# Kernel tuning notes

Hardware: AMD Instinct MI355X
Metric: run time of the kernel (lower is better)

The kernel has to match this reference:

```python
import jax, jax.numpy as jnp
import numpy as np

N_NODES = 100000


def _deg_inv_sqrt(dst, num_nodes):
    # degree with self-loops (PyG GCNConv default: add_self_loops=True)
    deg = jax.ops.segment_sum(jnp.ones(dst.shape[0], jnp.float32), dst,
                              num_segments=num_nodes) + 1.0
    return jax.lax.rsqrt(deg)


def gcn_conv(x, W, b, src, dst, dis, num_nodes):
    # PyG GCNConv: h = X W; out = D^-1/2 (A + I) D^-1/2 h + b
    h = x @ W                                  # [N, F_out]
    norm = dis[src] * dis[dst]                 # [E]
    msg = h[src] * norm[:, None]               # [E, F_out] (gather)
    out = jax.ops.segment_sum(msg, dst, num_segments=num_nodes)  # scatter-add
    out = out + h * (dis * dis)[:, None]       # self-loop contribution
    return out + b


def setup_inputs() -> dict:
    key = jax.random.key(0)
    ks = jax.random.split(key, 6)
    n, e = N_NODES, 1600000
    in_f, hid_f, out_f = 64, 64, 32
    x = jax.random.normal(ks[0], (n, in_f), jnp.float32)
    edge_index = jax.random.randint(ks[1], (2, e), 0, n, jnp.int64)
    s1 = 1.0 / np.sqrt(in_f)
    s2 = 1.0 / np.sqrt(hid_f)
    W1 = jax.random.normal(ks[2], (in_f, hid_f), jnp.float32) * s1
    b1 = jnp.zeros((hid_f,), jnp.float32)
    W2 = jax.random.normal(ks[3], (hid_f, out_f), jnp.float32) * s2
    b2 = jnp.zeros((out_f,), jnp.float32)
    return {"x": x, "edge_index": edge_index, "W1": W1, "b1": b1,
            "W2": W2, "b2": b2}


def reference(x, edge_index, W1, b1, W2, b2):
    src, dst = edge_index[0], edge_index[1]
    dis = _deg_inv_sqrt(dst, N_NODES)
    h = gcn_conv(x, W1, b1, src, dst, dis, N_NODES)
    h = jax.nn.relu(h)
    return gcn_conv(h, W2, b2, src, dst, dis, N_NODES)
```

## Files before the change

### kernel.cpp

```cpp
#include <hip/hip_runtime.h>
#include <hip/hip_bf16.h>


constexpr int N = 100000;
constexpr int E = 1600000;
constexpr int NBINS = 1563;
constexpr int HB    = 1568;
constexpr int CAP   = 1536;
constexpr int P1B   = 391;
constexpr int GB    = 1563;

__global__ void __launch_bounds__(256) fused_pass1_gemm1(
    const float* __restrict__ x, const float* __restrict__ W1,
    __hip_bfloat16* __restrict__ h1u,
    const int* __restrict__ src, const int* __restrict__ dst,
    int* __restrict__ cursor, unsigned* __restrict__ rec) {
    __shared__ float ws[64][64];
    __shared__ float xsT[64][64];
    const int bid = blockIdx.x;
    const int t = threadIdx.x;
    if (bid < P1B) {
        int* hist  = (int*)ws;
        int* rbase = hist + HB;
        int* rcur  = rbase + HB;
        for (int i = t; i < HB; i += 256) hist[i] = 0;
        __syncthreads();
        int myd[16], mys[16];
        const int e0 = bid * 4096;
#pragma unroll
        for (int it = 0; it < 16; ++it) {
            int idx = e0 + it * 256 + t;
            bool ok = idx < E;
            myd[it] = ok ? dst[idx] : -1;
            mys[it] = ok ? src[idx] : 0;
            if (ok) atomicAdd(&hist[myd[it] >> 6], 1);
        }
        __syncthreads();
        for (int i = t; i < HB; i += 256) {
            int h = hist[i];
            rbase[i] = (h > 0) ? atomicAdd(&cursor[i], h) : 0;
            rcur[i] = 0;
        }
        __syncthreads();
#pragma unroll
        for (int it = 0; it < 16; ++it) {
            if (myd[it] >= 0) {
                int cb = myd[it] >> 6;
                int r = atomicAdd(&rcur[cb], 1);
                int pos = rbase[cb] + r;
                if (pos < CAP)
                    rec[(size_t)cb * CAP + pos] =
                        ((unsigned)mys[it] << 6) | ((unsigned)myd[it] & 63u);
            }
        }
    } else {
        const int row0 = (bid - P1B) * 64;
        for (int i = t * 4; i < 64 * 64; i += 1024) {
            float4 v = *(const float4*)(W1 + i);
            ws[i >> 6][i & 63]       = v.x;
            ws[i >> 6][(i & 63) + 1] = v.y;
            ws[i >> 6][(i & 63) + 2] = v.z;
            ws[i >> 6][(i & 63) + 3] = v.w;
        }
        {
            const int r  = t & 63;
            const int k0 = (t >> 6) * 16;
            const int gr = row0 + r;
            if (gr < N) {
#pragma unroll
                for (int kk = 0; kk < 16; kk += 4) {
                    float4 v = *(const float4*)(x + (size_t)gr * 64 + k0 + kk);
                    xsT[k0 + kk][r]     = v.x;
                    xsT[k0 + kk + 1][r] = v.y;
                    xsT[k0 + kk + 2][r] = v.z;
                    xsT[k0 + kk + 3][r] = v.w;
                }
            } else {
#pragma unroll
                for (int kk = 0; kk < 16; ++kk) xsT[k0 + kk][r] = 0.0f;
            }
        }
        __syncthreads();
        const int c4 = (t & 15) * 4;
        const int r4 = (t >> 4) * 4;
        float acc[4][4];
#pragma unroll
        for (int i = 0; i < 4; ++i)
#pragma unroll
            for (int j = 0; j < 4; ++j) acc[i][j] = 0.0f;
#pragma unroll 4
        for (int k = 0; k < 64; ++k) {
            float4 wv = *(const float4*)&ws[k][c4];
            float4 xv = *(const float4*)&xsT[k][r4];
            float xa[4] = {xv.x, xv.y, xv.z, xv.w};
            float wa[4] = {wv.x, wv.y, wv.z, wv.w};
#pragma unroll
            for (int i = 0; i < 4; ++i)
#pragma unroll
                for (int j = 0; j < 4; ++j) acc[i][j] += xa[i] * wa[j];
        }
#pragma unroll
        for (int i = 0; i < 4; ++i) {
            const int gr = row0 + r4 + i;
            if (gr < N) {
                unsigned short o[4];
#pragma unroll
                for (int j = 0; j < 4; ++j)
                    o[j] = __bfloat16_as_ushort(__float2bfloat16(acc[i][j]));
                *(ushort4*)((unsigned short*)h1u + (size_t)gr * 64 + c4) =
                    *(const ushort4*)o;
            }
        }
    }
}

__global__ void __launch_bounds__(256) degree_kernel(
    const unsigned* __restrict__ rec, const int* __restrict__ cursor,
    float* __restrict__ dis) {
    __shared__ int cur[64];
    const int t = threadIdx.x;
    const int cb = blockIdx.x;
    if (t < 64) cur[t] = 0;
    __syncthreads();
    int m = cursor[cb];
    if (m > CAP) m = CAP;
    const unsigned* rb_ = rec + (size_t)cb * CAP;
    for (int i = t; i < m; i += 256)
        atomicAdd(&cur[rb_[i] & 63u], 1);
    __syncthreads();
    if (t < 64) {
        const int n = cb * 64 + t;
        if (n < N) dis[n] = rsqrtf((float)cur[t] + 1.0f);
    }
}

__device__ __forceinline__ void bf8_fma(float* acc, uint4 r, float w) {
    const unsigned u[4] = {r.x, r.y, r.z, r.w};
#pragma unroll
    for (int k = 0; k < 4; ++k) {
        acc[2 * k]     += __uint_as_float(u[k] << 16) * w;
        acc[2 * k + 1] += __uint_as_float(u[k] & 0xffff0000u) * w;
    }
}

__device__ __forceinline__ void bf8_acc(float* acc, uint4 r) {
    const unsigned u[4] = {r.x, r.y, r.z, r.w};
#pragma unroll
    for (int k = 0; k < 4; ++k) {
        acc[2 * k]     += __uint_as_float(u[k] << 16);
        acc[2 * k + 1] += __uint_as_float(u[k] & 0xffff0000u);
    }
}

__global__ void __launch_bounds__(512) agg1_fb(
    const __hip_bfloat16* __restrict__ h1u, const unsigned* __restrict__ rec,
    const int* __restrict__ cursor, const float* __restrict__ dis,
    const float* __restrict__ b, __hip_bfloat16* __restrict__ z1) {
    __shared__ unsigned lists[64 * 64];
    __shared__ int cur[64];
    const int t = threadIdx.x;
    const int cb = blockIdx.x;
    if (t < 64) cur[t] = 0;
    __syncthreads();
    int m = cursor[cb];
    if (m > CAP) m = CAP;
    const unsigned* rb_ = rec + (size_t)cb * CAP;
    for (int i = t; i < m; i += 512) {
        unsigned u = rb_[i];
        int dl = (int)(u & 63u);
        int r = atomicAdd(&cur[dl], 1);
        if (r < 64) lists[dl * 64 + r] = u >> 6;
    }
    __syncthreads();

    const unsigned short* hp = (const unsigned short*)h1u;
    const int row0 = cb * 64;
    const int nl = t >> 3;
    const int n = row0 + nl;
    const int fq = (t & 7) * 8;
    const int c = cur[nl];
    const int deg = (c < 64) ? c : 64;
    const unsigned* lp = &lists[nl * 64];
    float acc[8];
#pragma unroll
    for (int i = 0; i < 8; ++i) acc[i] = 0.0f;
    int j = 0;
    for (; j + 2 <= deg; j += 2) {
        unsigned s0 = lp[j], s1 = lp[j + 1];
        float w0 = dis[s0], w1 = dis[s1];
        uint4 r0 = *(const uint4*)(hp + (size_t)s0 * 64 + fq);
        uint4 r1 = *(const uint4*)(hp + (size_t)s1 * 64 + fq);
        bf8_fma(acc, r0, w0);
        bf8_fma(acc, r1, w1);
    }
    if (j < deg) {
        unsigned s0 = lp[j];
        float w0 = dis[s0];
        uint4 r0 = *(const uint4*)(hp + (size_t)s0 * 64 + fq);
        bf8_fma(acc, r0, w0);
    }
    if (n >= N) return;
    const float dn = rsqrtf((float)c + 1.0f);
    uint4 sr = *(const uint4*)(hp + (size_t)n * 64 + fq);
    bf8_fma(acc, sr, dn);
    float4 b0v = *(const float4*)(b + fq);
    float4 b1v = *(const float4*)(b + fq + 4);
    float bb[8] = {b0v.x, b0v.y, b0v.z, b0v.w, b1v.x, b1v.y, b1v.z, b1v.w};
    unsigned short o[8];
#pragma unroll
    for (int i = 0; i < 8; ++i) {
        float v = fmaxf(dn * acc[i] + bb[i], 0.0f);
        o[i] = __bfloat16_as_ushort(__float2bfloat16(v));
    }
    *(uint4*)((unsigned short*)z1 + (size_t)n * 64 + fq) = *(const uint4*)o;
}

__global__ void __launch_bounds__(256) gemm2_kernel(
    const __hip_bfloat16* __restrict__ Z, const float* __restrict__ W2,
    const float* __restrict__ dis, __hip_bfloat16* __restrict__ H2) {
    __shared__ float ws[64][32];
    __shared__ float xs[32][64];
    const int t = threadIdx.x;
    for (int i = t; i < 64 * 32; i += 256) ws[i >> 5][i & 31] = W2[i];
    const int row0 = blockIdx.x * 32;
    const unsigned short* Zp = (const unsigned short*)Z;
#pragma unroll
    for (int h = 0; h < 2; ++h) {
        int idx = h * 1024 + t * 4;
        int r = idx >> 6, k = idx & 63;
        ushort4 v = *(const ushort4*)(Zp + (size_t)(row0 + r) * 64 + k);
        xs[r][k]     = __uint_as_float((unsigned)v.x << 16);
        xs[r][k + 1] = __uint_as_float((unsigned)v.y << 16);
        xs[r][k + 2] = __uint_as_float((unsigned)v.z << 16);
        xs[r][k + 3] = __uint_as_float((unsigned)v.w << 16);
    }
    __syncthreads();
    const int c  = t & 31;
    const int rb = (t >> 5) * 4;
    float acc[4] = {0.f, 0.f, 0.f, 0.f};
    for (int k0 = 0; k0 < 64; k0 += 4) {
        float w0 = ws[k0][c], w1 = ws[k0 + 1][c];
        float w2 = ws[k0 + 2][c], w3 = ws[k0 + 3][c];
#pragma unroll
        for (int i = 0; i < 4; ++i) {
            float4 xv = *(const float4*)&xs[rb + i][k0];
            acc[i] += xv.x * w0;
            acc[i] += xv.y * w1;
            acc[i] += xv.z * w2;
            acc[i] += xv.w * w3;
        }
    }
#pragma unroll
    for (int i = 0; i < 4; ++i) {
        int row = row0 + rb + i;
        H2[(size_t)row * 32 + c] = __float2bfloat16(acc[i] * dis[row]);
    }
}

__global__ void __launch_bounds__(256) agg2_fb(
    const __hip_bfloat16* __restrict__ h2s, const unsigned* __restrict__ rec,
    const int* __restrict__ cursor, const float* __restrict__ b,
    float* __restrict__ out) {
    __shared__ unsigned lists[64 * 64];
    __shared__ int cur[64];
    const int t = threadIdx.x;
    const int cb = blockIdx.x;
    if (t < 64) cur[t] = 0;
    __syncthreads();
    int m = cursor[cb];
    if (m > CAP) m = CAP;
    const unsigned* rb_ = rec + (size_t)cb * CAP;
    for (int i = t; i < m; i += 256) {
        unsigned u = rb_[i];
        int dl = (int)(u & 63u);
        int r = atomicAdd(&cur[dl], 1);
        if (r < 64) lists[dl * 64 + r] = u >> 6;
    }
    __syncthreads();

    const unsigned short* hp = (const unsigned short*)h2s;
    const int row0 = cb * 64;
    const int nl = t >> 2;
    const int n = row0 + nl;
    const int fq = (t & 3) * 8;
    const int c = cur[nl];
    const int deg = (c < 64) ? c : 64;
    const unsigned* lp = &lists[nl * 64];
    float acc[8];
#pragma unroll
    for (int i = 0; i < 8; ++i) acc[i] = 0.0f;
    int j = 0;
    for (; j + 2 <= deg; j += 2) {
        unsigned s0 = lp[j], s1 = lp[j + 1];
        uint4 r0 = *(const uint4*)(hp + (size_t)s0 * 32 + fq);
        uint4 r1 = *(const uint4*)(hp + (size_t)s1 * 32 + fq);
        bf8_acc(acc, r0);
        bf8_acc(acc, r1);
    }
    if (j < deg) {
        unsigned s0 = lp[j];
        uint4 r0 = *(const uint4*)(hp + (size_t)s0 * 32 + fq);
        bf8_acc(acc, r0);
    }
    if (n >= N) return;
    uint4 sr = *(const uint4*)(hp + (size_t)n * 32 + fq);
    bf8_acc(acc, sr);
    const float dn = rsqrtf((float)c + 1.0f);
    float4 b0 = *(const float4*)(b + fq);
    float4 b1 = *(const float4*)(b + fq + 4);
    *(float4*)(out + (size_t)n * 32 + fq) =
        make_float4(dn * acc[0] + b0.x, dn * acc[1] + b0.y,
                    dn * acc[2] + b0.z, dn * acc[3] + b0.w);
    *(float4*)(out + (size_t)n * 32 + fq + 4) =
        make_float4(dn * acc[4] + b1.x, dn * acc[5] + b1.y,
                    dn * acc[6] + b1.z, dn * acc[7] + b1.w);
}

extern "C" void kernel_launch(void* const* d_in, const int* in_sizes, int n_in,
                              void* d_out, int out_size, void* d_ws, size_t ws_size,
                              hipStream_t stream) {
    const float* x  = (const float*)d_in[0];
    const int*   ei = (const int*)d_in[1];
    const float* W1 = (const float*)d_in[2];
    const float* b1 = (const float*)d_in[3];
    const float* W2 = (const float*)d_in[4];
    const float* b2 = (const float*)d_in[5];
    float* out = (float*)d_out;

    const int* src = ei;
    const int* dst = ei + E;

    constexpr size_t NP = 100352;
    int*      cursor = (int*)d_ws;
    float*    dis    = (float*)(cursor + 2048);
    unsigned* rec    = (unsigned*)(dis + NP);
    __hip_bfloat16* h1u = (__hip_bfloat16*)(rec + (size_t)NBINS * CAP);
    __hip_bfloat16* z1b = h1u + (size_t)N * 64;
    __hip_bfloat16* h2s = z1b + (size_t)N * 64;

    hipMemsetAsync(cursor, 0, 2048 * sizeof(int), stream);
    fused_pass1_gemm1<<<P1B + GB, 256, 0, stream>>>(x, W1, h1u, src, dst,
                                                    cursor, rec);
    degree_kernel<<<NBINS, 256, 0, stream>>>(rec, cursor, dis);
    agg1_fb<<<NBINS, 512, 0, stream>>>(h1u, rec, cursor, dis, b1, z1b);
    gemm2_kernel<<<N / 32, 256, 0, stream>>>(z1b, W2, dis, h2s);
    agg2_fb<<<NBINS, 256, 0, stream>>>(h2s, rec, cursor, b2, out);
}
```

Baseline: 185.1 us.

## Fuse layer-1 aggregation with the second GEMM into one half-bin kernel

Merges agg1 and gemm2 into one kernel. Each 256-thread block takes half of a 64-node bin, builds its neighbour lists, aggregates, applies ReLU into shared memory in fp32, then multiplies by W2 and writes the scaled bf16 h2. This removes the z1 round trip through global memory and one kernel launch. In exchange, every bin's record list is now scanned twice (once per half), and W2 is reloaded into shared memory by every block.

New measurement: 272.7 us. +47.3%, slower.

```diff
diff --git a/kernel.cpp b/kernel.cpp
--- a/kernel.cpp
+++ b/kernel.cpp
@@ -152,31 +152,40 @@
     }
 }
 
-__global__ void __launch_bounds__(512) agg1_fb(
+__global__ void __launch_bounds__(256) agg1_gemm2_half(
     const __hip_bfloat16* __restrict__ h1u, const unsigned* __restrict__ rec,
     const int* __restrict__ cursor, const float* __restrict__ dis,
-    const float* __restrict__ b, __hip_bfloat16* __restrict__ z1) {
-    __shared__ unsigned lists[64 * 64];
-    __shared__ int cur[64];
+    const float* __restrict__ b, const float* __restrict__ W2,
+    __hip_bfloat16* __restrict__ h2s) {
+    __shared__ float    ws[64][32];
+    __shared__ float    zs[32 * 68];
+    __shared__ unsigned lists[32 * 64];
+    __shared__ int      cur[32];
+    __shared__ float    dis_l[32];
     const int t = threadIdx.x;
-    const int cb = blockIdx.x;
-    if (t < 64) cur[t] = 0;
-    __syncthreads();
+    const int cb = blockIdx.x >> 1;
+    const int half = blockIdx.x & 1;
+    for (int i = t; i < 64 * 32; i += 256) ws[i >> 5][i & 31] = W2[i];
+    if (t < 32) cur[t] = 0;
+    __syncthreads();
+
     int m = cursor[cb];
     if (m > CAP) m = CAP;
     const unsigned* rb_ = rec + (size_t)cb * CAP;
-    for (int i = t; i < m; i += 512) {
+    const int hbase = half * 32;
+    for (int i = t; i < m; i += 256) {
         unsigned u = rb_[i];
-        int dl = (int)(u & 63u);
-        int r = atomicAdd(&cur[dl], 1);
-        if (r < 64) lists[dl * 64 + r] = u >> 6;
+        int dl = (int)(u & 63u) - hbase;
+        if ((unsigned)dl < 32u) {
+            int r = atomicAdd(&cur[dl], 1);
+            if (r < 64) lists[dl * 64 + r] = u >> 6;
+        }
     }
     __syncthreads();
 
     const unsigned short* hp = (const unsigned short*)h1u;
-    const int row0 = cb * 64;
     const int nl = t >> 3;
-    const int n = row0 + nl;
+    const int n = cb * 64 + hbase + nl;
     const int fq = (t & 7) * 8;
     const int c = cur[nl];
     const int deg = (c < 64) ? c : 64;
@@ -199,61 +208,48 @@
         uint4 r0 = *(const uint4*)(hp + (size_t)s0 * 64 + fq);
         bf8_fma(acc, r0, w0);
     }
-    if (n >= N) return;
-    const float dn = rsqrtf((float)c + 1.0f);
-    uint4 sr = *(const uint4*)(hp + (size_t)n * 64 + fq);
-    bf8_fma(acc, sr, dn);
-    float4 b0v = *(const float4*)(b + fq);
-    float4 b1v = *(const float4*)(b + fq + 4);
-    float bb[8] = {b0v.x, b0v.y, b0v.z, b0v.w, b1v.x, b1v.y, b1v.z, b1v.w};
-    unsigned short o[8];
-#pragma unroll
-    for (int i = 0; i < 8; ++i) {
-        float v = fmaxf(dn * acc[i] + bb[i], 0.0f);
-        o[i] = __bfloat16_as_ushort(__float2bfloat16(v));
-    }
-    *(uint4*)((unsigned short*)z1 + (size_t)n * 64 + fq) = *(const uint4*)o;
-}
-
-__global__ void __launch_bounds__(256) gemm2_kernel(
-    const __hip_bfloat16* __restrict__ Z, const float* __restrict__ W2,
-    const float* __restrict__ dis, __hip_bfloat16* __restrict__ H2) {
-    __shared__ float ws[64][32];
-    __shared__ float xs[32][64];
-    const int t = threadIdx.x;
-    for (int i = t; i < 64 * 32; i += 256) ws[i >> 5][i & 31] = W2[i];
-    const int row0 = blockIdx.x * 32;
-    const unsigned short* Zp = (const unsigned short*)Z;
-#pragma unroll
-    for (int h = 0; h < 2; ++h) {
-        int idx = h * 1024 + t * 4;
-        int r = idx >> 6, k = idx & 63;
-        ushort4 v = *(const ushort4*)(Zp + (size_t)(row0 + r) * 64 + k);
-        xs[r][k]     = __uint_as_float((unsigned)v.x << 16);
-        xs[r][k + 1] = __uint_as_float((unsigned)v.y << 16);
-        xs[r][k + 2] = __uint_as_float((unsigned)v.z << 16);
-        xs[r][k + 3] = __uint_as_float((unsigned)v.w << 16);
-    }
-    __syncthreads();
-    const int c  = t & 31;
-    const int rb = (t >> 5) * 4;
-    float acc[4] = {0.f, 0.f, 0.f, 0.f};
+    float* zr = &zs[nl * 68 + fq];
+    if (n < N) {
+        const float dn = rsqrtf((float)c + 1.0f);
+        uint4 sr = *(const uint4*)(hp + (size_t)n * 64 + fq);
+        bf8_fma(acc, sr, dn);
+        if ((t & 7) == 0) dis_l[nl] = dn;
+        float4 b0v = *(const float4*)(b + fq);
+        float4 b1v = *(const float4*)(b + fq + 4);
+        float bb[8] = {b0v.x, b0v.y, b0v.z, b0v.w, b1v.x, b1v.y, b1v.z, b1v.w};
+        float o[8];
+#pragma unroll
+        for (int i = 0; i < 8; ++i) o[i] = fmaxf(dn * acc[i] + bb[i], 0.0f);
+        *(float4*)(zr)     = make_float4(o[0], o[1], o[2], o[3]);
+        *(float4*)(zr + 4) = make_float4(o[4], o[5], o[6], o[7]);
+    } else {
+        *(float4*)(zr)     = make_float4(0.f, 0.f, 0.f, 0.f);
+        *(float4*)(zr + 4) = make_float4(0.f, 0.f, 0.f, 0.f);
+    }
+    __syncthreads();
+
+    const int cc = t & 31;
+    const int rbse = (t >> 5) * 4;
+    float oacc[4] = {0.f, 0.f, 0.f, 0.f};
     for (int k0 = 0; k0 < 64; k0 += 4) {
-        float w0 = ws[k0][c], w1 = ws[k0 + 1][c];
-        float w2 = ws[k0 + 2][c], w3 = ws[k0 + 3][c];
+        float w0 = ws[k0][cc], w1 = ws[k0 + 1][cc];
+        float w2 = ws[k0 + 2][cc], w3 = ws[k0 + 3][cc];
 #pragma unroll
         for (int i = 0; i < 4; ++i) {
-            float4 xv = *(const float4*)&xs[rb + i][k0];
-            acc[i] += xv.x * w0;
-            acc[i] += xv.y * w1;
-            acc[i] += xv.z * w2;
-            acc[i] += xv.w * w3;
+            float4 xv = *(const float4*)&zs[(rbse + i) * 68 + k0];
+            oacc[i] += xv.x * w0;
+            oacc[i] += xv.y * w1;
+            oacc[i] += xv.z * w2;
+            oacc[i] += xv.w * w3;
         }
     }
 #pragma unroll
     for (int i = 0; i < 4; ++i) {
-        int row = row0 + rb + i;
-        H2[(size_t)row * 32 + c] = __float2bfloat16(acc[i] * dis[row]);
+        const int row = cb * 64 + hbase + rbse + i;
+        if (row < N)
+            ((unsigned short*)h2s)[(size_t)row * 32 + cc] =
+                __bfloat16_as_ushort(
+                    __float2bfloat16(oacc[i] * dis_l[rbse + i]));
     }
 }
 
@@ -335,14 +331,13 @@
     float*    dis    = (float*)(cursor + 2048);
     unsigned* rec    = (unsigned*)(dis + NP);
     __hip_bfloat16* h1u = (__hip_bfloat16*)(rec + (size_t)NBINS * CAP);
-    __hip_bfloat16* z1b = h1u + (size_t)N * 64;
-    __hip_bfloat16* h2s = z1b + (size_t)N * 64;
+    __hip_bfloat16* h2s = h1u + (size_t)N * 64;
 
     hipMemsetAsync(cursor, 0, 2048 * sizeof(int), stream);
     fused_pass1_gemm1<<<P1B + GB, 256, 0, stream>>>(x, W1, h1u, src, dst,
                                                     cursor, rec);
     degree_kernel<<<NBINS, 256, 0, stream>>>(rec, cursor, dis);
-    agg1_fb<<<NBINS, 512, 0, stream>>>(h1u, rec, cursor, dis, b1, z1b);
-    gemm2_kernel<<<N / 32, 256, 0, stream>>>(z1b, W2, dis, h2s);
+    agg1_gemm2_half<<<2 * NBINS, 256, 0, stream>>>(h1u, rec, cursor, dis, b1,
+                                                   W2, h2s);
     agg2_fb<<<NBINS, 256, 0, stream>>>(h2s, rec, cursor, b2, out);
 }
```

## Fuse second-layer GEMM into first aggregation kernel via register partial dots and shuffles

Applied to the files above, without the earlier changes.

Merges the layer-1 aggregation with the layer-2 projection. Each group of 8 threads holds one node's 64 activated features and computes partial 32-wide dot products against W2 staged in shared memory, then reduces them with xor shuffles. This removes the z1 intermediate round trip to global memory and one kernel launch. In exchange it adds 32-element register arrays and redundant shuffle work, with register-pressure and occupancy risk under the new launch bounds.

Result: slower. 211.5 us (+14.3%).

```diff
diff --git a/kernel.cpp b/kernel.cpp
--- a/kernel.cpp
+++ b/kernel.cpp
@@ -152,14 +152,17 @@
     }
 }
 
-__global__ void __launch_bounds__(512) agg1_fb(
+__global__ void __launch_bounds__(512, 4) agg1_gemm2_reg(
     const __hip_bfloat16* __restrict__ h1u, const unsigned* __restrict__ rec,
     const int* __restrict__ cursor, const float* __restrict__ dis,
-    const float* __restrict__ b, __hip_bfloat16* __restrict__ z1) {
+    const float* __restrict__ b, const float* __restrict__ W2,
+    __hip_bfloat16* __restrict__ h2s) {
     __shared__ unsigned lists[64 * 64];
-    __shared__ int cur[64];
+    __shared__ float    ws[64][33];
+    __shared__ int      cur[64];
     const int t = threadIdx.x;
     const int cb = blockIdx.x;
+    for (int i = t; i < 2048; i += 512) ws[i >> 5][i & 31] = W2[i];
     if (t < 64) cur[t] = 0;
     __syncthreads();
     int m = cursor[cb];
@@ -177,7 +180,8 @@
     const int row0 = cb * 64;
     const int nl = t >> 3;
     const int n = row0 + nl;
-    const int fq = (t & 7) * 8;
+    const int l = t & 7;
+    const int fq = l * 8;
     const int c = cur[nl];
     const int deg = (c < 64) ? c : 64;
     const unsigned* lp = &lists[nl * 64];
@@ -206,55 +210,29 @@
     float4 b0v = *(const float4*)(b + fq);
     float4 b1v = *(const float4*)(b + fq + 4);
     float bb[8] = {b0v.x, b0v.y, b0v.z, b0v.w, b1v.x, b1v.y, b1v.z, b1v.w};
-    unsigned short o[8];
-#pragma unroll
-    for (int i = 0; i < 8; ++i) {
-        float v = fmaxf(dn * acc[i] + bb[i], 0.0f);
-        o[i] = __bfloat16_as_ushort(__float2bfloat16(v));
-    }
-    *(uint4*)((unsigned short*)z1 + (size_t)n * 64 + fq) = *(const uint4*)o;
-}
-
-__global__ void __launch_bounds__(256) gemm2_kernel(
-    const __hip_bfloat16* __restrict__ Z, const float* __restrict__ W2,
-    const float* __restrict__ dis, __hip_bfloat16* __restrict__ H2) {
-    __shared__ float ws[64][32];
-    __shared__ float xs[32][64];
-    const int t = threadIdx.x;
-    for (int i = t; i < 64 * 32; i += 256) ws[i >> 5][i & 31] = W2[i];
-    const int row0 = blockIdx.x * 32;
-    const unsigned short* Zp = (const unsigned short*)Z;
-#pragma unroll
-    for (int h = 0; h < 2; ++h) {
-        int idx = h * 1024 + t * 4;
-        int r = idx >> 6, k = idx & 63;
-        ushort4 v = *(const ushort4*)(Zp + (size_t)(row0 + r) * 64 + k);
-        xs[r][k]     = __uint_as_float((unsigned)v.x << 16);
-        xs[r][k + 1] = __uint_as_float((unsigned)v.y << 16);
-        xs[r][k + 2] = __uint_as_float((unsigned)v.z << 16);
-        xs[r][k + 3] = __uint_as_float((unsigned)v.w << 16);
-    }
-    __syncthreads();
-    const int c  = t & 31;
-    const int rb = (t >> 5) * 4;
-    float acc[4] = {0.f, 0.f, 0.f, 0.f};
-    for (int k0 = 0; k0 < 64; k0 += 4) {
-        float w0 = ws[k0][c], w1 = ws[k0 + 1][c];
-        float w2 = ws[k0 + 2][c], w3 = ws[k0 + 3][c];
-#pragma unroll
-        for (int i = 0; i < 4; ++i) {
-            float4 xv = *(const float4*)&xs[rb + i][k0];
-            acc[i] += xv.x * w0;
-            acc[i] += xv.y * w1;
-            acc[i] += xv.z * w2;
-            acc[i] += xv.w * w3;
-        }
-    }
-#pragma unroll
-    for (int i = 0; i < 4; ++i) {
-        int row = row0 + rb + i;
-        H2[(size_t)row * 32 + c] = __float2bfloat16(acc[i] * dis[row]);
-    }
+#pragma unroll
+    for (int i = 0; i < 8; ++i) acc[i] = fmaxf(dn * acc[i] + bb[i], 0.0f);
+
+    float p[32];
+#pragma unroll
+    for (int cc = 0; cc < 32; ++cc) {
+        float s = 0.0f;
+#pragma unroll
+        for (int i = 0; i < 8; ++i) s += acc[i] * ws[fq + i][cc];
+        p[cc] = s;
+    }
+#pragma unroll
+    for (int cc = 0; cc < 32; ++cc) {
+        p[cc] += __shfl_xor(p[cc], 1);
+        p[cc] += __shfl_xor(p[cc], 2);
+        p[cc] += __shfl_xor(p[cc], 4);
+    }
+    unsigned short o[4];
+#pragma unroll
+    for (int i = 0; i < 4; ++i)
+        o[i] = __bfloat16_as_ushort(__float2bfloat16(p[4 * l + i] * dn));
+    *(ushort4*)((unsigned short*)h2s + (size_t)n * 32 + 4 * l) =
+        *(const ushort4*)o;
 }
 
 __global__ void __launch_bounds__(256) agg2_fb(
@@ -335,14 +313,13 @@
     float*    dis    = (float*)(cursor + 2048);
     unsigned* rec    = (unsigned*)(dis + NP);
     __hip_bfloat16* h1u = (__hip_bfloat16*)(rec + (size_t)NBINS * CAP);
-    __hip_bfloat16* z1b = h1u + (size_t)N * 64;
-    __hip_bfloat16* h2s = z1b + (size_t)N * 64;
+    __hip_bfloat16* h2s = h1u + (size_t)N * 64;
 
     hipMemsetAsync(cursor, 0, 2048 * sizeof(int), stream);
     fused_pass1_gemm1<<<P1B + GB, 256, 0, stream>>>(x, W1, h1u, src, dst,
                                                     cursor, rec);
     degree_kernel<<<NBINS, 256, 0, stream>>>(rec, cursor, dis);
-    agg1_fb<<<NBINS, 512, 0, stream>>>(h1u, rec, cursor, dis, b1, z1b);
-    gemm2_kernel<<<N / 32, 256, 0, stream>>>(z1b, W2, dis, h2s);
+    agg1_gemm2_reg<<<NBINS, 512, 0, stream>>>(h1u, rec, cursor, dis, b1, W2,
+                                              h2s);
     agg2_fb<<<NBINS, 256, 0, stream>>>(h2s, rec, cursor, b2, out);
 }
```
